# Performance work log

Hardware: AMD Instinct MI355X
Metric: run time of the kernel (lower is better)

Reference implementation:

```python
import jax, jax.numpy as jnp
import numpy as np

H = 256    # hidden_size
B = 32     # batch_size (number of question groups)
NC = 5     # num_choices (5-way multiple choice)
TV = 2048  # max video length
TQ = 128   # max qa text length


def setup_inputs() -> dict:
    key = jax.random.key(0)
    ks = jax.random.split(key, 32)
    p = lambda i, shape: (0.01 * jax.random.normal(ks[i], shape)).astype(jnp.float32)
    z = lambda: jnp.zeros((H,), jnp.float32)
    return {
        "h": jax.random.normal(ks[0], (1, B * NC, H), dtype=jnp.float32),
        "hidden_frames": jax.random.normal(ks[1], (B * NC, TV, H), dtype=jnp.float32),
        "hidden_text": jax.random.normal(ks[2], (B * NC, TQ, H), dtype=jnp.float32),
        "Wav": p(3, (H, H)), "Wat": p(4, (H, H)),
        "Uav": p(5, (H, H)), "Uat": p(6, (H, H)),
        "Vav": p(7, (H,)), "Vat": p(8, (H,)),
        "bav": z(), "bat": z(),
        "Whh": p(9, (H, H)), "bh": z(),
        "Wvs": p(10, (H, H)), "bvs": z(),   # video_sum_encoder (W already transposed)
        "Wqs": p(11, (H, H)), "bqs": z(),   # question_sum_encoder
        "Wb": p(12, (H, H)),
        "Vbv": p(13, (H, H)), "Vbt": p(14, (H, H)),
        "bbv": z(), "bbt": z(),
        "wb": p(15, (H,)),
        "video_lens": jax.random.randint(ks[16], (B,), 1, TV + 1),
        "qa_lens": jax.random.randint(ks[17], (B * NC,), 1, TQ + 1),
        "batch_size": B,
        "num_choices": NC,
    }


def _masked_softmax(logits, mask):
    logits = jnp.where(mask, logits, jnp.float32(-1e30))
    return jax.nn.softmax(logits, axis=-1)


def _forward(h, hidden_frames, hidden_text, Wav, Wat, Uav, Uat, Vav, Vat, bav, bat,
             Whh, bh, Wvs, bvs, Wqs, bqs, Wb, Vbv, Vbt, bbv, bbt, wb,
             video_lens, qa_lens, batch_size, num_choices):
    Bn, Tv, Hd = hidden_frames.shape
    Tq = hidden_text.shape[1]
    Bb, nc = batch_size, num_choices
    hf = hidden_frames.reshape(Bb, nc, Tv, Hd)   # [B,nc,Tv,H]
    ht = hidden_text.reshape(Bb, nc, Tq, Hd)     # [B,nc,Tq,H]
    hh = h[0].reshape(Bb, nc, Hd)                # [B,nc,H]
    # per-group text length = max over the nc choices (matches original slicing)
    group_qal = qa_lens.reshape(Bb, nc).max(axis=1)                       # [B]
    vmask = jnp.arange(Tv)[None, None, :] < video_lens[:, None, None]    # [B,1,Tv]
    tmask = jnp.arange(Tq)[None, None, :] < group_qal[:, None, None]     # [B,1,Tq]
    # additive (Bahdanau) attention over video frames and text tokens
    Uhv = hh @ Uav                                                        # [B,nc,H]
    Uht = hh @ Uat
    ev = jnp.einsum('bnth,h->bnt', jnp.tanh(hf @ Wav + Uhv[:, :, None, :] + bav), Vav)
    et = jnp.einsum('bnth,h->bnt', jnp.tanh(ht @ Wat + Uht[:, :, None, :] + bat), Vat)
    av = _masked_softmax(ev, vmask)                                       # [B,nc,Tv]
    at = _masked_softmax(et, tmask)                                       # [B,nc,Tq]
    hv_sum = jnp.einsum('bnt,bnth->bnh', av, hf)                          # [B,nc,H]
    ht_sum = jnp.einsum('bnt,bnth->bnh', at, ht)
    hv_sum2 = hv_sum @ Wvs + bvs
    ht_sum2 = ht_sum @ Wqs + bqs
    # modality gating beta via 2-way softmax
    Wbs = hh @ Wb
    mv1 = hv_sum @ Vbv + bbv + Wbs
    mt1 = ht_sum @ Vbt + bbt + Wbs
    mtv = jnp.tanh(jnp.stack([mv1, mt1], axis=0))                         # [2,B,nc,H]
    beta = jax.nn.softmax(mtv @ wb, axis=0)                               # [2,B,nc]
    out = jnp.tanh(hh @ Whh + beta[0][..., None] * hv_sum2
                   + beta[1][..., None] * ht_sum2 + bh)                   # [B,nc,H]
    return out.reshape(Bb * nc, Hd)


def reference(h, hidden_frames, hidden_text, Wav, Wat, Uav, Uat, Vav, Vat, bav, bat,
              Whh, bh, Wvs, bvs, Wqs, bqs, Wb, Vbv, Vbt, bbv, bbt, wb,
              video_lens, qa_lens, batch_size, num_choices):
    return _forward(h, hidden_frames, hidden_text, Wav, Wat, Uav, Uat, Vav, Vat,
                    bav, bat, Whh, bh, Wvs, bvs, Wqs, bqs, Wb, Vbv, Vbt,
                    bbv, bbt, wb, video_lens, qa_lens, batch_size, num_choices)
```

## Files before the change

### kernel.cpp

```cpp
#include <hip/hip_runtime.h>

#define H   256
#define NCC 5
#define NBN 160
#define TVV 2048
#define TQQ 128

__device__ __forceinline__ float tanh_fast(float x) {
  x = fminf(fmaxf(x, -15.f), 15.f);
  float e = __expf(2.f * x);
  return (e - 1.f) / (e + 1.f);
}

__global__ __launch_bounds__(256) void k_prep(
    const float* __restrict__ h,
    const float* __restrict__ Uav, const float* __restrict__ Uat,
    const float* __restrict__ Wb,  const float* __restrict__ Whh,
    const float* __restrict__ bav, const float* __restrict__ bat,
    const float* __restrict__ bh,
    const int* __restrict__ video_lens, const int* __restrict__ qa_lens,
    float* __restrict__ Uhv, float* __restrict__ Uht,
    float* __restrict__ WbsA, float* __restrict__ HwhA,
    int* __restrict__ lenv, int* __restrict__ lent)
{
  const int bn = blockIdx.x, tid = threadIdx.x;
  __shared__ float hs[H];
  hs[tid] = h[bn * H + tid];
  __syncthreads();
  float a0 = bav[tid], a1 = bat[tid], a2 = 0.f, a3 = bh[tid];
#pragma unroll 4
  for (int k = 0; k < H; ++k) {
    const float x = hs[k];
    a0 = fmaf(x, Uav[k * H + tid], a0);
    a1 = fmaf(x, Uat[k * H + tid], a1);
    a2 = fmaf(x, Wb [k * H + tid], a2);
    a3 = fmaf(x, Whh[k * H + tid], a3);
  }
  Uhv [bn * H + tid] = a0;
  Uht [bn * H + tid] = a1;
  WbsA[bn * H + tid] = a2;
  HwhA[bn * H + tid] = a3;
  if (tid == 0) {
    const int b = bn / NCC;
    lenv[bn] = video_lens[b];
    int m = qa_lens[b * NCC];
    for (int j = 1; j < NCC; ++j) {
      int q = qa_lens[b * NCC + j];
      m = (q > m) ? q : m;
    }
    lent[bn] = m;
  }
}

__global__ __launch_bounds__(256) void k_logits(
    const float* __restrict__ X,
    const float* __restrict__ W,
    const float* __restrict__ U,
    const float* __restrict__ Vv,
    const int*  __restrict__ lenp,
    int T,
    float* __restrict__ EV)
{
  const int bn = blockIdx.y;
  const int t0 = blockIdx.x * 64;
  const int len = lenp[bn];
  if (t0 >= len) return;

  const int tid = threadIdx.x;
  const int hg = tid & 31;
  const int tg = tid >> 5;

  __shared__ float Ws[32][H];
  __shared__ float AsT[32][72];

  float acc[8][8];
#pragma unroll
  for (int i = 0; i < 8; ++i)
#pragma unroll
    for (int j = 0; j < 8; ++j) acc[i][j] = 0.f;

  const float* Xrow = X + ((size_t)bn * T + t0) * H;

  for (int k0 = 0; k0 < H; k0 += 32) {
    __syncthreads();
    {
      const int r = tid >> 6;
      const int c = (tid & 63) * 4;
#pragma unroll
      for (int i = 0; i < 8; ++i) {
        const float4 w = *(const float4*)&W[(size_t)(k0 + r + i * 4) * H + c];
        *(float4*)&Ws[r + i * 4][c] = w;
      }
    }
    {
      const int ti = tid >> 2;
      const int kq = (tid & 3) * 8;
      const float4 v0 = *(const float4*)&Xrow[(size_t)ti * H + k0 + kq];
      const float4 v1 = *(const float4*)&Xrow[(size_t)ti * H + k0 + kq + 4];
      AsT[kq + 0][ti] = v0.x; AsT[kq + 1][ti] = v0.y;
      AsT[kq + 2][ti] = v0.z; AsT[kq + 3][ti] = v0.w;
      AsT[kq + 4][ti] = v1.x; AsT[kq + 5][ti] = v1.y;
      AsT[kq + 6][ti] = v1.z; AsT[kq + 7][ti] = v1.w;
    }
    __syncthreads();
#pragma unroll 4
    for (int k = 0; k < 32; ++k) {
      const float4 a0 = *(const float4*)&AsT[k][tg * 8];
      const float4 a1 = *(const float4*)&AsT[k][tg * 8 + 4];
      const float4 b0 = *(const float4*)&Ws[k][hg * 8];
      const float4 b1 = *(const float4*)&Ws[k][hg * 8 + 4];
      const float av_[8] = {a0.x, a0.y, a0.z, a0.w, a1.x, a1.y, a1.z, a1.w};
      const float bv_[8] = {b0.x, b0.y, b0.z, b0.w, b1.x, b1.y, b1.z, b1.w};
#pragma unroll
      for (int i = 0; i < 8; ++i)
#pragma unroll
        for (int j = 0; j < 8; ++j)
          acc[i][j] = fmaf(av_[i], bv_[j], acc[i][j]);
    }
  }

  float u[8], vv[8];
#pragma unroll
  for (int j = 0; j < 8; ++j) {
    u[j]  = U[bn * H + hg * 8 + j];
    vv[j] = Vv[hg * 8 + j];
  }
#pragma unroll
  for (int i = 0; i < 8; ++i) {
    float p = 0.f;
#pragma unroll
    for (int j = 0; j < 8; ++j) p = fmaf(tanh_fast(acc[i][j] + u[j]), vv[j], p);
    p += __shfl_xor(p, 16);
    p += __shfl_xor(p, 8);
    p += __shfl_xor(p, 4);
    p += __shfl_xor(p, 2);
    p += __shfl_xor(p, 1);
    if (hg == 0) EV[(size_t)bn * T + t0 + tg * 8 + i] = p;
  }
}

template <int T>
__global__ __launch_bounds__(256) void k_softmax_pv(
    const float* __restrict__ EV,
    const float* __restrict__ X,
    const int*  __restrict__ lenp,
    float* __restrict__ OUT)
{
  const int bn = blockIdx.x, tid = threadIdx.x;
  const int len = lenp[bn];
  __shared__ float pl[T];
  __shared__ float red[8];
  const float* ev = EV + (size_t)bn * T;

  float m = -1e30f;
  for (int t = tid; t < len; t += 256) m = fmaxf(m, ev[t]);
  for (int off = 32; off; off >>= 1) m = fmaxf(m, __shfl_xor(m, off));
  if ((tid & 63) == 0) red[tid >> 6] = m;
  __syncthreads();
  m = fmaxf(fmaxf(red[0], red[1]), fmaxf(red[2], red[3]));

  float s = 0.f;
  for (int t = tid; t < len; t += 256) {
    const float p = __expf(ev[t] - m);
    pl[t] = p;
    s += p;
  }
  for (int off = 32; off; off >>= 1) s += __shfl_xor(s, off);
  if ((tid & 63) == 0) red[4 + (tid >> 6)] = s;
  __syncthreads();
  s = red[4] + red[5] + red[6] + red[7];
  const float inv = 1.f / s;

  const float* Xb = X + (size_t)bn * T * H;
  float acc = 0.f;
  int t = 0;
  for (; t + 8 <= len; t += 8) {
#pragma unroll
    for (int j = 0; j < 8; ++j)
      acc = fmaf(pl[t + j], Xb[(size_t)(t + j) * H + tid], acc);
  }
  for (; t < len; ++t) acc = fmaf(pl[t], Xb[(size_t)t * H + tid], acc);
  OUT[bn * H + tid] = acc * inv;
}

__global__ __launch_bounds__(256) void k_final(
    const float* __restrict__ HVS, const float* __restrict__ HTS,
    const float* __restrict__ Wvs, const float* __restrict__ bvs,
    const float* __restrict__ Wqs, const float* __restrict__ bqs,
    const float* __restrict__ Vbv, const float* __restrict__ Vbt,
    const float* __restrict__ bbv, const float* __restrict__ bbt,
    const float* __restrict__ wb,
    const float* __restrict__ WbsA, const float* __restrict__ HwhA,
    float* __restrict__ out)
{
  const int bn = blockIdx.x, tid = threadIdx.x;
  __shared__ float hv[H], ht[H];
  __shared__ float red[8];
  hv[tid] = HVS[bn * H + tid];
  ht[tid] = HTS[bn * H + tid];
  __syncthreads();

  const float wbs = WbsA[bn * H + tid];
  float hv2 = bvs[tid], ht2 = bqs[tid];
  float mv = bbv[tid] + wbs, mt = bbt[tid] + wbs;
#pragma unroll 4
  for (int k = 0; k < H; ++k) {
    const float a = hv[k], c = ht[k];
    hv2 = fmaf(a, Wvs[k * H + tid], hv2);
    ht2 = fmaf(c, Wqs[k * H + tid], ht2);
    mv  = fmaf(a, Vbv[k * H + tid], mv);
    mt  = fmaf(c, Vbt[k * H + tid], mt);
  }
  const float w = wb[tid];
  float sv = tanh_fast(mv) * w;
  float st = tanh_fast(mt) * w;
  for (int off = 32; off; off >>= 1) {
    sv += __shfl_xor(sv, off);
    st += __shfl_xor(st, off);
  }
  if ((tid & 63) == 0) { red[tid >> 6] = sv; red[4 + (tid >> 6)] = st; }
  __syncthreads();
  sv = red[0] + red[1] + red[2] + red[3];
  st = red[4] + red[5] + red[6] + red[7];
  const float mx = fmaxf(sv, st);
  const float e0 = __expf(sv - mx), e1 = __expf(st - mx);
  const float den = 1.f / (e0 + e1);
  out[bn * H + tid] = tanh_fast(HwhA[bn * H + tid] + (e0 * den) * hv2 + (e1 * den) * ht2);
}

extern "C" void kernel_launch(void* const* d_in, const int* in_sizes, int n_in,
                              void* d_out, int out_size, void* d_ws, size_t ws_size,
                              hipStream_t stream) {
  const float* h   = (const float*)d_in[0];
  const float* hf  = (const float*)d_in[1];
  const float* htx = (const float*)d_in[2];
  const float* Wav = (const float*)d_in[3];
  const float* Wat = (const float*)d_in[4];
  const float* Uav = (const float*)d_in[5];
  const float* Uat = (const float*)d_in[6];
  const float* Vav = (const float*)d_in[7];
  const float* Vat = (const float*)d_in[8];
  const float* bav = (const float*)d_in[9];
  const float* bat = (const float*)d_in[10];
  const float* Whh = (const float*)d_in[11];
  const float* bh  = (const float*)d_in[12];
  const float* Wvs = (const float*)d_in[13];
  const float* bvs = (const float*)d_in[14];
  const float* Wqs = (const float*)d_in[15];
  const float* bqs = (const float*)d_in[16];
  const float* Wb  = (const float*)d_in[17];
  const float* Vbv = (const float*)d_in[18];
  const float* Vbt = (const float*)d_in[19];
  const float* bbv = (const float*)d_in[20];
  const float* bbt = (const float*)d_in[21];
  const float* wb  = (const float*)d_in[22];
  const int* video_lens = (const int*)d_in[23];
  const int* qa_lens    = (const int*)d_in[24];

  float* ws   = (float*)d_ws;
  float* Uhv  = ws;
  float* Uht  = Uhv  + NBN * H;
  float* WbsA = Uht  + NBN * H;
  float* HwhA = WbsA + NBN * H;
  float* HVS  = HwhA + NBN * H;
  float* HTS  = HVS  + NBN * H;
  float* EVb  = HTS  + NBN * H;
  float* ETb  = EVb  + (size_t)NBN * TVV;
  int*   lenv = (int*)(ETb + (size_t)NBN * TQQ);
  int*   lent = lenv + NBN;

  k_prep<<<NBN, 256, 0, stream>>>(h, Uav, Uat, Wb, Whh, bav, bat, bh,
                                  video_lens, qa_lens, Uhv, Uht, WbsA, HwhA,
                                  lenv, lent);
  k_logits<<<dim3(TVV / 64, NBN), 256, 0, stream>>>(hf, Wav, Uhv, Vav, lenv, TVV, EVb);
  k_logits<<<dim3(TQQ / 64, NBN), 256, 0, stream>>>(htx, Wat, Uht, Vat, lent, TQQ, ETb);
  k_softmax_pv<TVV><<<NBN, 256, 0, stream>>>(EVb, hf, lenv, HVS);
  k_softmax_pv<TQQ><<<NBN, 256, 0, stream>>>(ETb, htx, lent, HTS);
  k_final<<<NBN, 256, 0, stream>>>(HVS, HTS, Wvs, bvs, Wqs, bqs, Vbv, Vbt,
                                   bbv, bbt, wb, WbsA, HwhA, (float*)d_out);
}
```

Baseline: 1.031 ms.

## Use bf16 MFMA for attention logits and split video softmax-PV across blocks

Replaces the FP32 SIMT tiled GEMM in the logits kernel with bf16 MFMA 16x16x32 instructions. The weights are pre-transposed and converted to bf16 by a new kernel, and activations are converted on the fly. The video softmax-weighted sum is split into a stats kernel and a multi-block PV kernel that accumulates with atomics, which raises parallelism over the long video axis. This lowers compute cost and the single-block-per-sequence bottleneck, at the price of bf16 precision loss in the logits and nondeterministic atomic accumulation order.

```diff
diff --git a/kernel.cpp b/kernel.cpp
--- a/kernel.cpp
+++ b/kernel.cpp
@@ -6,10 +6,40 @@
 #define TVV 2048
 #define TQQ 128
 
+typedef short bf16x8 __attribute__((ext_vector_type(8)));
+typedef float f32x4  __attribute__((ext_vector_type(4)));
+
 __device__ __forceinline__ float tanh_fast(float x) {
   x = fminf(fmaxf(x, -15.f), 15.f);
   float e = __expf(2.f * x);
   return (e - 1.f) / (e + 1.f);
+}
+
+__device__ __forceinline__ short f2b(float f) {
+  union { float f; unsigned u; } v; v.f = f;
+  return (short)((v.u + 0x7fffu + ((v.u >> 16) & 1u)) >> 16);
+}
+
+__global__ __launch_bounds__(256) void k_wt(
+    const float* __restrict__ W0, const float* __restrict__ W1,
+    short* __restrict__ T0, short* __restrict__ T1)
+{
+  const float* W = blockIdx.z ? W1 : W0;
+  short* Wt = blockIdx.z ? T1 : T0;
+  __shared__ float t[32][33];
+  const int k0 = blockIdx.y * 32, h0 = blockIdx.x * 32;
+  const int tx = threadIdx.x & 31, ty = threadIdx.x >> 5;
+#pragma unroll
+  for (int i = 0; i < 4; ++i) {
+    const int k = ty + i * 8;
+    t[k][tx] = W[(size_t)(k0 + k) * H + h0 + tx];
+  }
+  __syncthreads();
+#pragma unroll
+  for (int i = 0; i < 4; ++i) {
+    const int hh = ty + i * 8;
+    Wt[(size_t)(h0 + hh) * H + k0 + tx] = f2b(t[tx][hh]);
+  }
 }
 
 __global__ __launch_bounds__(256) void k_prep(
@@ -52,99 +82,132 @@
   }
 }
 
-__global__ __launch_bounds__(256) void k_logits(
+__global__ __launch_bounds__(256) void k_logits_mfma(
     const float* __restrict__ X,
-    const float* __restrict__ W,
+    const short* __restrict__ Wt,
     const float* __restrict__ U,
     const float* __restrict__ Vv,
     const int*  __restrict__ lenp,
     int T,
     float* __restrict__ EV)
 {
-  const int bn = blockIdx.y;
-  const int t0 = blockIdx.x * 64;
+  const int bn  = blockIdx.y;
+  const int len = lenp[bn];
+  const int tid = threadIdx.x;
+  const int wid = tid >> 6;
+  const int t0  = blockIdx.x * 64 + wid * 16;
+  if (t0 >= len) return;
+  const int lane = tid & 63;
+  const int li = lane & 15;
+  const int kg = lane >> 4;
+
+  const float* Xr = X + ((size_t)bn * T + t0 + li) * H + kg * 8;
+  const short* Wr = Wt + li * H + kg * 8;
+
+  f32x4 acc[16];
+  const f32x4 zero = {0.f, 0.f, 0.f, 0.f};
+#pragma unroll
+  for (int ct = 0; ct < 16; ++ct) acc[ct] = zero;
+
+#pragma unroll 2
+  for (int k0 = 0; k0 < H; k0 += 32) {
+    const float4 x0 = *(const float4*)(Xr + k0);
+    const float4 x1 = *(const float4*)(Xr + k0 + 4);
+    bf16x8 a;
+    a[0] = f2b(x0.x); a[1] = f2b(x0.y); a[2] = f2b(x0.z); a[3] = f2b(x0.w);
+    a[4] = f2b(x1.x); a[5] = f2b(x1.y); a[6] = f2b(x1.z); a[7] = f2b(x1.w);
+    const short* wp = Wr + k0;
+#pragma unroll
+    for (int ct = 0; ct < 16; ++ct) {
+      const bf16x8 b = *(const bf16x8*)(wp + ct * 16 * H);
+      acc[ct] = __builtin_amdgcn_mfma_f32_16x16x32_bf16(a, b, acc[ct], 0, 0, 0);
+    }
+  }
+
+  float p0 = 0.f, p1 = 0.f, p2 = 0.f, p3 = 0.f;
+#pragma unroll
+  for (int ct = 0; ct < 16; ++ct) {
+    const int hh = ct * 16 + li;
+    const float u = U[bn * H + hh];
+    const float v = Vv[hh];
+    p0 = fmaf(tanh_fast(acc[ct][0] + u), v, p0);
+    p1 = fmaf(tanh_fast(acc[ct][1] + u), v, p1);
+    p2 = fmaf(tanh_fast(acc[ct][2] + u), v, p2);
+    p3 = fmaf(tanh_fast(acc[ct][3] + u), v, p3);
+  }
+#pragma unroll
+  for (int m = 1; m < 16; m <<= 1) {
+    p0 += __shfl_xor(p0, m); p1 += __shfl_xor(p1, m);
+    p2 += __shfl_xor(p2, m); p3 += __shfl_xor(p3, m);
+  }
+  if (li == 0) {
+    float* e = EV + (size_t)bn * T + t0 + kg * 4;
+    e[0] = p0; e[1] = p1; e[2] = p2; e[3] = p3;
+  }
+}
+
+__global__ __launch_bounds__(256) void k_smax(
+    const float* __restrict__ EV, const int* __restrict__ lenp,
+    float* __restrict__ stats, float* __restrict__ ACC)
+{
+  const int bn = blockIdx.x, tid = threadIdx.x;
+  const int len = lenp[bn];
+  const float* ev = EV + (size_t)bn * TVV;
+  __shared__ float red[8];
+
+  float m = -1e30f;
+  for (int t = tid; t < len; t += 256) m = fmaxf(m, ev[t]);
+  for (int off = 32; off; off >>= 1) m = fmaxf(m, __shfl_xor(m, off));
+  if ((tid & 63) == 0) red[tid >> 6] = m;
+  __syncthreads();
+  m = fmaxf(fmaxf(red[0], red[1]), fmaxf(red[2], red[3]));
+
+  float s = 0.f;
+  for (int t = tid; t < len; t += 256) s += __expf(ev[t] - m);
+  for (int off = 32; off; off >>= 1) s += __shfl_xor(s, off);
+  if ((tid & 63) == 0) red[4 + (tid >> 6)] = s;
+  __syncthreads();
+  if (tid == 0) {
+    s = red[4] + red[5] + red[6] + red[7];
+    stats[bn * 2]     = m;
+    stats[bn * 2 + 1] = 1.f / s;
+  }
+  ACC[bn * H + tid] = 0.f;
+}
+
+__global__ __launch_bounds__(256) void k_pv(
+    const float* __restrict__ EV, const float* __restrict__ X,
+    const int* __restrict__ lenp, const float* __restrict__ stats,
+    float* __restrict__ ACC)
+{
+  const int bn = blockIdx.y, tid = threadIdx.x;
+  const int t0 = blockIdx.x * 256;
   const int len = lenp[bn];
   if (t0 >= len) return;
-
-  const int tid = threadIdx.x;
-  const int hg = tid & 31;
-  const int tg = tid >> 5;
-
-  __shared__ float Ws[32][H];
-  __shared__ float AsT[32][72];
-
-  float acc[8][8];
-#pragma unroll
-  for (int i = 0; i < 8; ++i)
-#pragma unroll
-    for (int j = 0; j < 8; ++j) acc[i][j] = 0.f;
-
-  const float* Xrow = X + ((size_t)bn * T + t0) * H;
-
-  for (int k0 = 0; k0 < H; k0 += 32) {
-    __syncthreads();
-    {
-      const int r = tid >> 6;
-      const int c = (tid & 63) * 4;
-#pragma unroll
-      for (int i = 0; i < 8; ++i) {
-        const float4 w = *(const float4*)&W[(size_t)(k0 + r + i * 4) * H + c];
-        *(float4*)&Ws[r + i * 4][c] = w;
-      }
-    }
-    {
-      const int ti = tid >> 2;
-      const int kq = (tid & 3) * 8;
-      const float4 v0 = *(const float4*)&Xrow[(size_t)ti * H + k0 + kq];
-      const float4 v1 = *(const float4*)&Xrow[(size_t)ti * H + k0 + kq + 4];
-      AsT[kq + 0][ti] = v0.x; AsT[kq + 1][ti] = v0.y;
-      AsT[kq + 2][ti] = v0.z; AsT[kq + 3][ti] = v0.w;
-      AsT[kq + 4][ti] = v1.x; AsT[kq + 5][ti] = v1.y;
-      AsT[kq + 6][ti] = v1.z; AsT[kq + 7][ti] = v1.w;
-    }
-    __syncthreads();
-#pragma unroll 4
-    for (int k = 0; k < 32; ++k) {
-      const float4 a0 = *(const float4*)&AsT[k][tg * 8];
-      const float4 a1 = *(const float4*)&AsT[k][tg * 8 + 4];
-      const float4 b0 = *(const float4*)&Ws[k][hg * 8];
-      const float4 b1 = *(const float4*)&Ws[k][hg * 8 + 4];
-      const float av_[8] = {a0.x, a0.y, a0.z, a0.w, a1.x, a1.y, a1.z, a1.w};
-      const float bv_[8] = {b0.x, b0.y, b0.z, b0.w, b1.x, b1.y, b1.z, b1.w};
-#pragma unroll
-      for (int i = 0; i < 8; ++i)
-#pragma unroll
-        for (int j = 0; j < 8; ++j)
-          acc[i][j] = fmaf(av_[i], bv_[j], acc[i][j]);
-    }
-  }
-
-  float u[8], vv[8];
-#pragma unroll
-  for (int j = 0; j < 8; ++j) {
-    u[j]  = U[bn * H + hg * 8 + j];
-    vv[j] = Vv[hg * 8 + j];
-  }
-#pragma unroll
-  for (int i = 0; i < 8; ++i) {
-    float p = 0.f;
-#pragma unroll
-    for (int j = 0; j < 8; ++j) p = fmaf(tanh_fast(acc[i][j] + u[j]), vv[j], p);
-    p += __shfl_xor(p, 16);
-    p += __shfl_xor(p, 8);
-    p += __shfl_xor(p, 4);
-    p += __shfl_xor(p, 2);
-    p += __shfl_xor(p, 1);
-    if (hg == 0) EV[(size_t)bn * T + t0 + tg * 8 + i] = p;
-  }
+  const float m = stats[bn * 2], inv = stats[bn * 2 + 1];
+
+  __shared__ float pl[256];
+  const int t = t0 + tid;
+  pl[tid] = (t < len) ? __expf(EV[(size_t)bn * TVV + t] - m) * inv : 0.f;
+  __syncthreads();
+
+  const int lim = min(256, len - t0);
+  const float* Xb = X + ((size_t)bn * TVV + t0) * H;
+  float acc = 0.f;
+  int j = 0;
+  for (; j + 8 <= lim; j += 8) {
+#pragma unroll
+    for (int u = 0; u < 8; ++u)
+      acc = fmaf(pl[j + u], Xb[(size_t)(j + u) * H + tid], acc);
+  }
+  for (; j < lim; ++j) acc = fmaf(pl[j], Xb[(size_t)j * H + tid], acc);
+  atomicAdd(&ACC[bn * H + tid], acc);
 }
 
 template <int T>
 __global__ __launch_bounds__(256) void k_softmax_pv(
-    const float* __restrict__ EV,
-    const float* __restrict__ X,
-    const int*  __restrict__ lenp,
-    float* __restrict__ OUT)
+    const float* __restrict__ EV, const float* __restrict__ X,
+    const int* __restrict__ lenp, float* __restrict__ OUT)
 {
   const int bn = blockIdx.x, tid = threadIdx.x;
   const int len = lenp[bn];
@@ -257,24 +320,29 @@
   const int* video_lens = (const int*)d_in[23];
   const int* qa_lens    = (const int*)d_in[24];
 
-  float* ws   = (float*)d_ws;
-  float* Uhv  = ws;
-  float* Uht  = Uhv  + NBN * H;
-  float* WbsA = Uht  + NBN * H;
-  float* HwhA = WbsA + NBN * H;
-  float* HVS  = HwhA + NBN * H;
-  float* HTS  = HVS  + NBN * H;
-  float* EVb  = HTS  + NBN * H;
-  float* ETb  = EVb  + (size_t)NBN * TVV;
-  int*   lenv = (int*)(ETb + (size_t)NBN * TQQ);
-  int*   lent = lenv + NBN;
-
+  float* ws    = (float*)d_ws;
+  float* Uhv   = ws;
+  float* Uht   = Uhv  + NBN * H;
+  float* WbsA  = Uht  + NBN * H;
+  float* HwhA  = WbsA + NBN * H;
+  float* HVS   = HwhA + NBN * H;
+  float* HTS   = HVS  + NBN * H;
+  float* EVb   = HTS  + NBN * H;
+  float* ETb   = EVb  + (size_t)NBN * TVV;
+  float* stats = ETb  + (size_t)NBN * TQQ;
+  int*   lenv  = (int*)(stats + NBN * 2);
+  int*   lent  = lenv + NBN;
+  short* Wtv   = (short*)(lent + NBN);
+  short* Wtt   = Wtv + H * H;
+
+  k_wt<<<dim3(8, 8, 2), 256, 0, stream>>>(Wav, Wat, Wtv, Wtt);
   k_prep<<<NBN, 256, 0, stream>>>(h, Uav, Uat, Wb, Whh, bav, bat, bh,
                                   video_lens, qa_lens, Uhv, Uht, WbsA, HwhA,
                                   lenv, lent);
-  k_logits<<<dim3(TVV / 64, NBN), 256, 0, stream>>>(hf, Wav, Uhv, Vav, lenv, TVV, EVb);
-  k_logits<<<dim3(TQQ / 64, NBN), 256, 0, stream>>>(htx, Wat, Uht, Vat, lent, TQQ, ETb);
-  k_softmax_pv<TVV><<<NBN, 256, 0, stream>>>(EVb, hf, lenv, HVS);
+  k_logits_mfma<<<dim3(TVV / 64, NBN), 256, 0, stream>>>(hf, Wtv, Uhv, Vav, lenv, TVV, EVb);
+  k_logits_mfma<<<dim3(TQQ / 64, NBN), 256, 0, stream>>>(htx, Wtt, Uht, Vat, lent, TQQ, ETb);
+  k_smax<<<NBN, 256, 0, stream>>>(EVb, lenv, stats, HVS);
+  k_pv<<<dim3(TVV / 256, NBN), 256, 0, stream>>>(EVb, hf, lenv, stats, HVS);
   k_softmax_pv<TQQ><<<NBN, 256, 0, stream>>>(ETb, htx, lent, HTS);
   k_final<<<NBN, 256, 0, stream>>>(HVS, HTS, Wvs, bvs, Wqs, bqs, Vbv, Vbt,
                                    bbv, bbt, wb, WbsA, HwhA, (float*)d_out);
```

New measurement: 890.7 us. 13.6% less time.
